# Performance work log

Measured on AMD Instinct MI355X. Metric: run time of the kernel, lower is better.

The kernel has to match this reference:

```python
import jax, jax.numpy as jnp
import numpy as np

ROI = 7      # pooled output size
S = 5        # max adaptive samples per bin dim (boxes <= 0.25*120=30px -> ceil(30/7)=5)


def _roi_align(f, boxes):
    """torchvision roi_align, aligned=True, sampling_ratio=-1 (adaptive).
    f: [C,H,W]; boxes: [N,4] normalized xywh. Returns [N,C,ROI,ROI]."""
    C, H, W = f.shape
    fH, fW = jnp.float32(H), jnp.float32(W)
    x1 = boxes[:, 0] * fW - 0.5                 # aligned=True offset
    y1 = boxes[:, 1] * fH - 0.5
    roi_w = boxes[:, 2] * fW
    roi_h = boxes[:, 3] * fH
    bin_w = roi_w / ROI
    bin_h = roi_h / ROI
    gw = jnp.maximum(jnp.ceil(roi_w / ROI), 1.0)   # adaptive grid counts [N]
    gh = jnp.maximum(jnp.ceil(roi_h / ROI), 1.0)
    ph = jnp.arange(ROI, dtype=jnp.float32)
    s = jnp.arange(S, dtype=jnp.float32)
    # sample coords [N, ROI, S]
    ys = y1[:, None, None] + ph[None, :, None] * bin_h[:, None, None] \
         + (s[None, None, :] + 0.5) * bin_h[:, None, None] / gh[:, None, None]
    xs = x1[:, None, None] + ph[None, :, None] * bin_w[:, None, None] \
         + (s[None, None, :] + 0.5) * bin_w[:, None, None] / gw[:, None, None]
    # broadcast to [N, ROI, ROI, S, S]
    y = ys[:, :, None, :, None]
    x = xs[:, None, :, None, :]
    m = ((s[None, None, None, :, None] < gh[:, None, None, None, None]) &
         (s[None, None, None, None, :] < gw[:, None, None, None, None]))
    valid = (y > -1.0) & (y < fH) & (x > -1.0) & (x < fW)
    yc = jnp.clip(y, 0.0, fH - 1.0)
    xc = jnp.clip(x, 0.0, fW - 1.0)
    y0 = jnp.floor(yc).astype(jnp.int32)
    x0 = jnp.floor(xc).astype(jnp.int32)
    yh = jnp.minimum(y0 + 1, H - 1)
    xh = jnp.minimum(x0 + 1, W - 1)
    ly = yc - y0.astype(jnp.float32); hy = 1.0 - ly
    lx = xc - x0.astype(jnp.float32); hx = 1.0 - lx
    scale = (valid & m).astype(f.dtype)
    y = jnp.broadcast_to(y0 * 0, (boxes.shape[0], ROI, ROI, S, S))  # shape anchor (unused)
    w00 = (hy * hx * scale)[None]
    w01 = (hy * lx * scale)[None]
    w10 = (ly * hx * scale)[None]
    w11 = (ly * lx * scale)[None]
    # gathered values: [C, N, ROI, ROI, S, S]
    vals = (w00 * f[:, y0, x0] + w01 * f[:, y0, xh] +
            w10 * f[:, yh, x0] + w11 * f[:, yh, xh])
    count = (gh * gw)[None, :, None, None]
    pooled = vals.sum(axis=(-1, -2)) / count        # [C, N, ROI, ROI]
    return pooled.transpose(1, 0, 2, 3)              # [N, C, ROI, ROI]


def setup_inputs() -> dict:
    key = jax.random.key(0)
    k = jax.random.split(key, 6)
    features = jax.random.normal(k[0], (1, 128, 120, 120), jnp.float32)
    u = jax.random.uniform(k[1], (512, 4), jnp.float32)
    boxes = jnp.stack([u[:, 0] * 0.7, u[:, 1] * 0.7,
                       0.05 + 0.2 * u[:, 2], 0.05 + 0.2 * u[:, 3]], axis=1)
    d_in = 128 * ROI * ROI  # 6272
    W1 = jax.random.normal(k[2], (d_in, 512), jnp.float32) / np.float32(np.sqrt(d_in))
    b1 = jax.random.normal(k[3], (512,), jnp.float32) * 0.01
    W2 = jax.random.normal(k[4], (512, 256), jnp.float32) / np.float32(np.sqrt(512))
    b2 = jax.random.normal(k[5], (256,), jnp.float32) * 0.01
    return {"features": features, "boxes": boxes, "W1": W1, "b1": b1, "W2": W2, "b2": b2}


def reference(features, boxes, W1, b1, W2, b2):
    roi = _roi_align(features[0], boxes)             # [N,128,7,7]
    flat = roi.reshape(roi.shape[0], -1)             # [N,6272] channel-major like torch .view
    h = jax.nn.relu(flat @ W1 + b1)                  # dropout in eval mode = identity
    return h @ W2 + b2                               # [N,256]
```

## Files before the change

### kernel.cpp

```cpp
#include <hip/hip_runtime.h>
#include <hip/hip_bf16.h>
#include <stdint.h>

#define DI __device__ __forceinline__

typedef __attribute__((ext_vector_type(8))) short short8;
typedef __attribute__((ext_vector_type(4))) float f32x4;

constexpr int CH   = 128;
constexpr int FH   = 120;
constexpr int FW   = 120;
constexpr int NBOX = 512;
constexpr int KDIM = 49 * 128;
constexpr int D1   = 512;
constexpr int D2   = 256;
constexpr int SPLITS = 14;
constexpr int KC     = KDIM / SPLITS;

DI float bf2f(uint32_t u16) { union { uint32_t i; float f; } v; v.i = u16 << 16; return v.f; }
DI float bf2f_hi(uint32_t u) { union { uint32_t i; float f; } v; v.i = u & 0xffff0000u; return v.f; }
DI uint16_t f2bf(float f) {
    __hip_bfloat16 h = __float2bfloat16(f);
    union { __hip_bfloat16 h; uint16_t u; } v; v.h = h; return v.u;
}

__global__ __launch_bounds__(256) void k_pre(const float* __restrict__ f,
                                             const float* __restrict__ W1,
                                             const float* __restrict__ W2,
                                             uint32_t* __restrict__ ft,
                                             uint16_t* __restrict__ W1rT,
                                             uint16_t* __restrict__ W2T) {
    __shared__ __align__(16) char smem[16896];
    const int v = blockIdx.x, t = threadIdx.x;
    if (v < 480) {
        float* lds = (float*)smem;
        const int y = v >> 2, x0 = (v & 3) * 30;
        for (int e = t; e < 30 * 128; e += 256) {
            int c = e / 30, x = e - c * 30;
            lds[x * 129 + c] = f[c * (FH * FW) + y * FW + x0 + x];
        }
        __syncthreads();
        for (int e = t; e < 30 * 64; e += 256) {
            int x = e >> 6, cp = e & 63;
            float lo = lds[x * 129 + 2 * cp];
            float hi = lds[x * 129 + 2 * cp + 1];
            ft[(y * FW + x0 + x) * 64 + cp] = (uint32_t)f2bf(lo) | ((uint32_t)f2bf(hi) << 16);
        }
    } else if (v < 512) {
        float* lds = (float*)smem;
        const int v2 = v - 480;
        const int n0 = (v2 & 7) * 32, k0 = (v2 >> 3) * 128;
        for (int e = t; e < 4096; e += 256) {
            int k = e >> 5, nn = e & 31;
            lds[k * 33 + nn] = W2[(k0 + k) * D2 + n0 + nn];
        }
        __syncthreads();
        for (int e = t; e < 4096; e += 256) {
            int nn = e >> 7, k = e & 127;
            W2T[(n0 + nn) * D1 + k0 + k] = f2bf(lds[k * 33 + nn]);
        }
    } else {
        float* lds = (float*)smem;
        const int vb = v - 512;
        const int b = vb % 49, j0 = (vb / 49) * 32;
        for (int e = t; e < 4096; e += 256) {
            int ci = e >> 5, jj = e & 31;
            lds[ci * 33 + jj] = W1[(ci * 49 + b) * D1 + j0 + jj];
        }
        __syncthreads();
        for (int e = t; e < 4096; e += 256) {
            int jj = e >> 7, ci = e & 127;
            W1rT[(size_t)(j0 + jj) * KDIM + b * 128 + ci] = f2bf(lds[ci * 33 + jj]);
        }
    }
}

__global__ __launch_bounds__(256) void k_roi(const uint32_t* __restrict__ ft,
                                             const float* __restrict__ boxes,
                                             uint32_t* __restrict__ A) {
#pragma clang fp contract(off)
    const int wid  = (blockIdx.x << 2) + (threadIdx.x >> 6);
    const int lane = threadIdx.x & 63;
    const int box = wid / 49, bin = wid % 49;
    const int ph = bin / 7, pw = bin % 7;

    const float bx = boxes[box * 4 + 0], by = boxes[box * 4 + 1];
    const float bw = boxes[box * 4 + 2], bh = boxes[box * 4 + 3];
    const float x1 = bx * 120.0f - 0.5f;
    const float y1 = by * 120.0f - 0.5f;
    const float roi_w = bw * 120.0f, roi_h = bh * 120.0f;
    const float bin_w = roi_w / 7.0f, bin_h = roi_h / 7.0f;
    const float gwf = fmaxf(ceilf(roi_w / 7.0f), 1.0f);
    const float ghf = fmaxf(ceilf(roi_h / 7.0f), 1.0f);
    const int gwi = (int)gwf, ghi = (int)ghf;

    const float ybase = y1 + (float)ph * bin_h;
    const float xbase = x1 + (float)pw * bin_w;

    int offx0[5], offxh[5];
    float hxm[5], lxm[5];
#pragma unroll
    for (int j = 0; j < 5; ++j) {
        float xx = xbase + ((float)j + 0.5f) * bin_w / gwf;
        bool vx = (j < gwi) && (xx > -1.0f) && (xx < 120.0f);
        float xc = fminf(fmaxf(xx, 0.0f), 119.0f);
        int x0 = (int)floorf(xc);
        int xh = min(x0 + 1, 119);
        float lx = xc - (float)x0, hx = 1.0f - lx;
        float mx = vx ? 1.0f : 0.0f;
        hxm[j] = hx * mx; lxm[j] = lx * mx;
        offx0[j] = x0 * 64; offxh[j] = xh * 64;
    }

    float acc0 = 0.0f, acc1 = 0.0f;
    for (int sy = 0; sy < ghi; ++sy) {
        float yy = ybase + ((float)sy + 0.5f) * bin_h / ghf;
        float my = ((yy > -1.0f) && (yy < 120.0f)) ? 1.0f : 0.0f;
        float yc = fminf(fmaxf(yy, 0.0f), 119.0f);
        int y0 = (int)floorf(yc);
        int yh = min(y0 + 1, 119);
        float ly = yc - (float)y0, hy = 1.0f - ly;
        float hym = hy * my, lym = ly * my;
        const uint32_t* r0 = ft + (size_t)(y0 * FW) * 64 + lane;
        const uint32_t* r1 = ft + (size_t)(yh * FW) * 64 + lane;
        uint32_t u00[5], u01[5], u10[5], u11[5];
#pragma unroll
        for (int j = 0; j < 5; ++j) {
            u00[j] = r0[offx0[j]];
            u01[j] = r0[offxh[j]];
            u10[j] = r1[offx0[j]];
            u11[j] = r1[offxh[j]];
        }
#pragma unroll
        for (int j = 0; j < 5; ++j) {
            float w00 = hym * hxm[j], w01 = hym * lxm[j];
            float w10 = lym * hxm[j], w11 = lym * lxm[j];
            acc0 += w00 * bf2f(u00[j] & 0xffffu) + w01 * bf2f(u01[j] & 0xffffu)
                  + w10 * bf2f(u10[j] & 0xffffu) + w11 * bf2f(u11[j] & 0xffffu);
            acc1 += w00 * bf2f_hi(u00[j]) + w01 * bf2f_hi(u01[j])
                  + w10 * bf2f_hi(u10[j]) + w11 * bf2f_hi(u11[j]);
        }
    }
    const float cnt = ghf * gwf;
    const float v0 = acc0 / cnt, v1 = acc1 / cnt;
    A[(size_t)wid * 64 + lane] = (uint32_t)f2bf(v0) | ((uint32_t)f2bf(v1) << 16);
}

__global__ __launch_bounds__(256) void k_gemm1(const uint16_t* __restrict__ A,
                                               const uint16_t* __restrict__ B,
                                               float* __restrict__ P) {
    __shared__ __align__(16) uint16_t As[128 * 32];
    __shared__ __align__(16) uint16_t Bs[128 * 32];
    const int t = threadIdx.x;
    const int lane = t & 63, w = t >> 6;
    const int wr = w >> 1, wc = w & 1;
    const int m0 = blockIdx.x * 128, n0 = blockIdx.y * 128;
    const int kbase = blockIdx.z * KC;

    f32x4 acc[4][4] = {};
    const int kb = lane >> 4, r16 = lane & 15;

    for (int ks = 0; ks < KC / 32; ++ks) {
        const int kk = kbase + ks * 32;
        __syncthreads();
#pragma unroll
        for (int i = 0; i < 2; ++i) {
            int ch = t + 256 * i;
            int row = ch >> 2, c8 = ch & 3;
            int sw = (row >> 1) & 3;
            const uint16_t* ga = A + (size_t)(m0 + row) * KDIM + kk + c8 * 8;
            *(uint4*)&As[row * 32 + (c8 ^ sw) * 8] = *(const uint4*)ga;
            const uint16_t* gb = B + (size_t)(n0 + row) * KDIM + kk + c8 * 8;
            *(uint4*)&Bs[row * 32 + (c8 ^ sw) * 8] = *(const uint4*)gb;
        }
        __syncthreads();

        short8 af[4], bfr[4];
#pragma unroll
        for (int mi = 0; mi < 4; ++mi) {
            int ar = wr * 64 + mi * 16 + r16;
            af[mi] = *(const short8*)&As[ar * 32 + (kb ^ ((ar >> 1) & 3)) * 8];
        }
#pragma unroll
        for (int ni = 0; ni < 4; ++ni) {
            int br = wc * 64 + ni * 16 + r16;
            bfr[ni] = *(const short8*)&Bs[br * 32 + (kb ^ ((br >> 1) & 3)) * 8];
        }
#pragma unroll
        for (int mi = 0; mi < 4; ++mi)
#pragma unroll
            for (int ni = 0; ni < 4; ++ni)
                acc[mi][ni] = __builtin_amdgcn_mfma_f32_16x16x32_bf16(af[mi], bfr[ni], acc[mi][ni], 0, 0, 0);
    }

    float* outp = P + (size_t)blockIdx.z * (D1 * D1);
#pragma unroll
    for (int mi = 0; mi < 4; ++mi)
#pragma unroll
        for (int ni = 0; ni < 4; ++ni) {
            int row = m0 + wr * 64 + mi * 16 + kb * 4;
            int col = n0 + wc * 64 + ni * 16 + r16;
#pragma unroll
            for (int r = 0; r < 4; ++r)
                outp[(size_t)(row + r) * D1 + col] = acc[mi][ni][r];
        }
}

__global__ __launch_bounds__(256) void k_reduce1(const float* __restrict__ P,
                                                 const float* __restrict__ b1,
                                                 uint16_t* __restrict__ Hm) {
    const int e4 = blockIdx.x * 256 + threadIdx.x;
    const f32x4* P4 = (const f32x4*)P;
    f32x4 s = {};
#pragma unroll
    for (int i = 0; i < SPLITS; ++i) s += P4[(size_t)i * (D1 * D1 / 4) + e4];
    const int c4 = (e4 & 127) * 4;
    uint16_t h[4];
#pragma unroll
    for (int j = 0; j < 4; ++j) h[j] = f2bf(fmaxf(s[j] + b1[c4 + j], 0.0f));
    uint2 pk;
    pk.x = (uint32_t)h[0] | ((uint32_t)h[1] << 16);
    pk.y = (uint32_t)h[2] | ((uint32_t)h[3] << 16);
    *(uint2*)&Hm[(size_t)e4 * 4] = pk;
}

__global__ __launch_bounds__(256) void k_gemm2(const uint16_t* __restrict__ Hm,
                                               const uint16_t* __restrict__ W2T,
                                               const float* __restrict__ b2,
                                               float* __restrict__ out) {
    const int wid  = blockIdx.x * 4 + (threadIdx.x >> 6);
    const int lane = threadIdx.x & 63;
    const int mt = wid >> 4, nt = wid & 15;
    const int m0 = mt * 16, n0 = nt * 16;
    const int g = lane >> 4, i = lane & 15;
    f32x4 acc = {};
#pragma unroll
    for (int kk = 0; kk < D1 / 32; ++kk) {
        short8 a = *(const short8*)&Hm[(m0 + i) * D1 + kk * 32 + g * 8];
        short8 b = *(const short8*)&W2T[(n0 + i) * D1 + kk * 32 + g * 8];
        acc = __builtin_amdgcn_mfma_f32_16x16x32_bf16(a, b, acc, 0, 0, 0);
    }
    const float bias = b2[n0 + i];
#pragma unroll
    for (int r = 0; r < 4; ++r)
        out[(size_t)(m0 + g * 4 + r) * D2 + n0 + i] = acc[r] + bias;
}

extern "C" void kernel_launch(void* const* d_in, const int* in_sizes, int n_in,
                              void* d_out, int out_size, void* d_ws, size_t ws_size,
                              hipStream_t stream) {
    const float* f     = (const float*)d_in[0];
    const float* boxes = (const float*)d_in[1];
    const float* W1    = (const float*)d_in[2];
    const float* b1    = (const float*)d_in[3];
    const float* W2    = (const float*)d_in[4];
    const float* b2    = (const float*)d_in[5];
    float* out = (float*)d_out;

    char* p = (char*)d_ws;
    uint32_t* ft   = (uint32_t*)p; p += (size_t)FH * FW * (CH / 2) * 4;
    uint16_t* W1rT = (uint16_t*)p; p += (size_t)D1 * KDIM * 2;
    uint16_t* W2T  = (uint16_t*)p; p += (size_t)D2 * D1 * 2;
    uint16_t* Ar   = (uint16_t*)p; p += (size_t)NBOX * KDIM * 2;
    float*    Pp   = (float*)p;    p += (size_t)SPLITS * D1 * D1 * 4;
    uint16_t* Hm   = (uint16_t*)p; p += (size_t)D1 * D1 * 2;

    k_pre<<<1296, 256, 0, stream>>>(f, W1, W2, ft, W1rT, W2T);
    k_roi<<<(NBOX * 49) / 4, 256, 0, stream>>>(ft, boxes, (uint32_t*)Ar);
    k_gemm1<<<dim3(4, 4, SPLITS), 256, 0, stream>>>(Ar, W1rT, Pp);
    k_reduce1<<<D1 * D1 / 4 / 256, 256, 0, stream>>>(Pp, b1, Hm);
    k_gemm2<<<(D1 / 16) * (D2 / 16) / 4, 256, 0, stream>>>(Hm, W2T, b2, out);
}
```

Measured before the change: 70.70 us.

## Move weight conversion into ROI kernel and fuse split-K reduce into GEMM2

The weight transpose/convert blocks for W1 and W2 move out of the preprocessing kernel and into the ROI-align launch as extra blocks. Preprocessing now only transposes the feature map, which shortens the critical path before ROI sampling. The split-K reduction with bias and ReLU is fused into the second GEMM through LDS, which removes one launch and the Hm round trip to global memory. The fused GEMM2 runs only 32 blocks, so the split-K reduction gets less parallelism than before.

```diff
diff --git a/kernel.cpp b/kernel.cpp
--- a/kernel.cpp
+++ b/kernel.cpp
@@ -24,31 +24,114 @@
     union { __hip_bfloat16 h; uint16_t u; } v; v.h = h; return v.u;
 }
 
-__global__ __launch_bounds__(256) void k_pre(const float* __restrict__ f,
-                                             const float* __restrict__ W1,
-                                             const float* __restrict__ W2,
-                                             uint32_t* __restrict__ ft,
-                                             uint16_t* __restrict__ W1rT,
-                                             uint16_t* __restrict__ W2T) {
-    __shared__ __align__(16) char smem[16896];
+__global__ __launch_bounds__(256) void k_preft(const float* __restrict__ f,
+                                               uint32_t* __restrict__ ft) {
+    __shared__ float lds[30 * 129];
     const int v = blockIdx.x, t = threadIdx.x;
-    if (v < 480) {
-        float* lds = (float*)smem;
-        const int y = v >> 2, x0 = (v & 3) * 30;
-        for (int e = t; e < 30 * 128; e += 256) {
-            int c = e / 30, x = e - c * 30;
-            lds[x * 129 + c] = f[c * (FH * FW) + y * FW + x0 + x];
-        }
-        __syncthreads();
-        for (int e = t; e < 30 * 64; e += 256) {
-            int x = e >> 6, cp = e & 63;
-            float lo = lds[x * 129 + 2 * cp];
-            float hi = lds[x * 129 + 2 * cp + 1];
-            ft[(y * FW + x0 + x) * 64 + cp] = (uint32_t)f2bf(lo) | ((uint32_t)f2bf(hi) << 16);
-        }
-    } else if (v < 512) {
-        float* lds = (float*)smem;
-        const int v2 = v - 480;
+    const int y = v >> 2, x0 = (v & 3) * 30;
+    for (int e = t; e < 30 * 128; e += 256) {
+        int c = e / 30, x = e - c * 30;
+        lds[x * 129 + c] = f[c * (FH * FW) + y * FW + x0 + x];
+    }
+    __syncthreads();
+    for (int e = t; e < 30 * 64; e += 256) {
+        int x = e >> 6, cp = e & 63;
+        float lo = lds[x * 129 + 2 * cp];
+        float hi = lds[x * 129 + 2 * cp + 1];
+        ft[(y * FW + x0 + x) * 64 + cp] = (uint32_t)f2bf(lo) | ((uint32_t)f2bf(hi) << 16);
+    }
+}
+
+__global__ __launch_bounds__(256) void k_roi_w(const uint32_t* __restrict__ ft,
+                                               const float* __restrict__ boxes,
+                                               const float* __restrict__ W1,
+                                               const float* __restrict__ W2,
+                                               uint32_t* __restrict__ A,
+                                               uint16_t* __restrict__ W1rT,
+                                               uint16_t* __restrict__ W2T) {
+    __shared__ __align__(16) float lds[128 * 33];
+    const int blk = blockIdx.x, t = threadIdx.x;
+    if (blk < 6272) {
+#pragma clang fp contract(off)
+        const int wid  = (blk << 2) + (t >> 6);
+        const int lane = t & 63;
+        const int box = wid / 49, bin = wid % 49;
+        const int ph = bin / 7, pw = bin % 7;
+
+        const float bx = boxes[box * 4 + 0], by = boxes[box * 4 + 1];
+        const float bw = boxes[box * 4 + 2], bh = boxes[box * 4 + 3];
+        const float x1 = bx * 120.0f - 0.5f;
+        const float y1 = by * 120.0f - 0.5f;
+        const float roi_w = bw * 120.0f, roi_h = bh * 120.0f;
+        const float bin_w = roi_w / 7.0f, bin_h = roi_h / 7.0f;
+        const float gwf = fmaxf(ceilf(roi_w / 7.0f), 1.0f);
+        const float ghf = fmaxf(ceilf(roi_h / 7.0f), 1.0f);
+        const int gwi = (int)gwf, ghi = (int)ghf;
+
+        const float ybase = y1 + (float)ph * bin_h;
+        const float xbase = x1 + (float)pw * bin_w;
+
+        int offx0[5], offxh[5];
+        float hxm[5], lxm[5];
+#pragma unroll
+        for (int j = 0; j < 5; ++j) {
+            float xx = xbase + ((float)j + 0.5f) * bin_w / gwf;
+            bool vx = (j < gwi) && (xx > -1.0f) && (xx < 120.0f);
+            float xc = fminf(fmaxf(xx, 0.0f), 119.0f);
+            int x0 = (int)floorf(xc);
+            int xh = min(x0 + 1, 119);
+            float lx = xc - (float)x0, hx = 1.0f - lx;
+            float mx = vx ? 1.0f : 0.0f;
+            hxm[j] = hx * mx; lxm[j] = lx * mx;
+            offx0[j] = x0 * 64; offxh[j] = xh * 64;
+        }
+
+        float acc0 = 0.0f, acc1 = 0.0f;
+        for (int sy = 0; sy < ghi; ++sy) {
+            float yy = ybase + ((float)sy + 0.5f) * bin_h / ghf;
+            float my = ((yy > -1.0f) && (yy < 120.0f)) ? 1.0f : 0.0f;
+            float yc = fminf(fmaxf(yy, 0.0f), 119.0f);
+            int y0 = (int)floorf(yc);
+            int yh = min(y0 + 1, 119);
+            float ly = yc - (float)y0, hy = 1.0f - ly;
+            float hym = hy * my, lym = ly * my;
+            const uint32_t* r0 = ft + (size_t)(y0 * FW) * 64 + lane;
+            const uint32_t* r1 = ft + (size_t)(yh * FW) * 64 + lane;
+            uint32_t u00[5], u01[5], u10[5], u11[5];
+#pragma unroll
+            for (int j = 0; j < 5; ++j) {
+                u00[j] = r0[offx0[j]];
+                u01[j] = r0[offxh[j]];
+                u10[j] = r1[offx0[j]];
+                u11[j] = r1[offxh[j]];
+            }
+#pragma unroll
+            for (int j = 0; j < 5; ++j) {
+                float w00 = hym * hxm[j], w01 = hym * lxm[j];
+                float w10 = lym * hxm[j], w11 = lym * lxm[j];
+                acc0 += w00 * bf2f(u00[j] & 0xffffu) + w01 * bf2f(u01[j] & 0xffffu)
+                      + w10 * bf2f(u10[j] & 0xffffu) + w11 * bf2f(u11[j] & 0xffffu);
+                acc1 += w00 * bf2f_hi(u00[j]) + w01 * bf2f_hi(u01[j])
+                      + w10 * bf2f_hi(u10[j]) + w11 * bf2f_hi(u11[j]);
+            }
+        }
+        const float cnt = ghf * gwf;
+        const float v0 = acc0 / cnt, v1 = acc1 / cnt;
+        A[(size_t)wid * 64 + lane] = (uint32_t)f2bf(v0) | ((uint32_t)f2bf(v1) << 16);
+    } else if (blk < 7056) {
+        const int vb = blk - 6272;
+        const int b = vb % 49, j0 = (vb / 49) * 32;
+        for (int e = t; e < 4096; e += 256) {
+            int ci = e >> 5, jj = e & 31;
+            lds[ci * 33 + jj] = W1[(ci * 49 + b) * D1 + j0 + jj];
+        }
+        __syncthreads();
+        for (int e = t; e < 4096; e += 256) {
+            int jj = e >> 7, ci = e & 127;
+            W1rT[(size_t)(j0 + jj) * KDIM + b * 128 + ci] = f2bf(lds[ci * 33 + jj]);
+        }
+    } else {
+        const int v2 = blk - 7056;
         const int n0 = (v2 & 7) * 32, k0 = (v2 >> 3) * 128;
         for (int e = t; e < 4096; e += 256) {
             int k = e >> 5, nn = e & 31;
@@ -59,91 +142,7 @@
             int nn = e >> 7, k = e & 127;
             W2T[(n0 + nn) * D1 + k0 + k] = f2bf(lds[k * 33 + nn]);
         }
-    } else {
-        float* lds = (float*)smem;
-        const int vb = v - 512;
-        const int b = vb % 49, j0 = (vb / 49) * 32;
-        for (int e = t; e < 4096; e += 256) {
-            int ci = e >> 5, jj = e & 31;
-            lds[ci * 33 + jj] = W1[(ci * 49 + b) * D1 + j0 + jj];
-        }
-        __syncthreads();
-        for (int e = t; e < 4096; e += 256) {
-            int jj = e >> 7, ci = e & 127;
-            W1rT[(size_t)(j0 + jj) * KDIM + b * 128 + ci] = f2bf(lds[ci * 33 + jj]);
-        }
-    }
-}
-
-__global__ __launch_bounds__(256) void k_roi(const uint32_t* __restrict__ ft,
-                                             const float* __restrict__ boxes,
-                                             uint32_t* __restrict__ A) {
-#pragma clang fp contract(off)
-    const int wid  = (blockIdx.x << 2) + (threadIdx.x >> 6);
-    const int lane = threadIdx.x & 63;
-    const int box = wid / 49, bin = wid % 49;
-    const int ph = bin / 7, pw = bin % 7;
-
-    const float bx = boxes[box * 4 + 0], by = boxes[box * 4 + 1];
-    const float bw = boxes[box * 4 + 2], bh = boxes[box * 4 + 3];
-    const float x1 = bx * 120.0f - 0.5f;
-    const float y1 = by * 120.0f - 0.5f;
-    const float roi_w = bw * 120.0f, roi_h = bh * 120.0f;
-    const float bin_w = roi_w / 7.0f, bin_h = roi_h / 7.0f;
-    const float gwf = fmaxf(ceilf(roi_w / 7.0f), 1.0f);
-    const float ghf = fmaxf(ceilf(roi_h / 7.0f), 1.0f);
-    const int gwi = (int)gwf, ghi = (int)ghf;
-
-    const float ybase = y1 + (float)ph * bin_h;
-    const float xbase = x1 + (float)pw * bin_w;
-
-    int offx0[5], offxh[5];
-    float hxm[5], lxm[5];
-#pragma unroll
-    for (int j = 0; j < 5; ++j) {
-        float xx = xbase + ((float)j + 0.5f) * bin_w / gwf;
-        bool vx = (j < gwi) && (xx > -1.0f) && (xx < 120.0f);
-        float xc = fminf(fmaxf(xx, 0.0f), 119.0f);
-        int x0 = (int)floorf(xc);
-        int xh = min(x0 + 1, 119);
-        float lx = xc - (float)x0, hx = 1.0f - lx;
-        float mx = vx ? 1.0f : 0.0f;
-        hxm[j] = hx * mx; lxm[j] = lx * mx;
-        offx0[j] = x0 * 64; offxh[j] = xh * 64;
-    }
-
-    float acc0 = 0.0f, acc1 = 0.0f;
-    for (int sy = 0; sy < ghi; ++sy) {
-        float yy = ybase + ((float)sy + 0.5f) * bin_h / ghf;
-        float my = ((yy > -1.0f) && (yy < 120.0f)) ? 1.0f : 0.0f;
-        float yc = fminf(fmaxf(yy, 0.0f), 119.0f);
-        int y0 = (int)floorf(yc);
-        int yh = min(y0 + 1, 119);
-        float ly = yc - (float)y0, hy = 1.0f - ly;
-        float hym = hy * my, lym = ly * my;
-        const uint32_t* r0 = ft + (size_t)(y0 * FW) * 64 + lane;
-        const uint32_t* r1 = ft + (size_t)(yh * FW) * 64 + lane;
-        uint32_t u00[5], u01[5], u10[5], u11[5];
-#pragma unroll
-        for (int j = 0; j < 5; ++j) {
-            u00[j] = r0[offx0[j]];
-            u01[j] = r0[offxh[j]];
-            u10[j] = r1[offx0[j]];
-            u11[j] = r1[offxh[j]];
-        }
-#pragma unroll
-        for (int j = 0; j < 5; ++j) {
-            float w00 = hym * hxm[j], w01 = hym * lxm[j];
-            float w10 = lym * hxm[j], w11 = lym * lxm[j];
-            acc0 += w00 * bf2f(u00[j] & 0xffffu) + w01 * bf2f(u01[j] & 0xffffu)
-                  + w10 * bf2f(u10[j] & 0xffffu) + w11 * bf2f(u11[j] & 0xffffu);
-            acc1 += w00 * bf2f_hi(u00[j]) + w01 * bf2f_hi(u01[j])
-                  + w10 * bf2f_hi(u10[j]) + w11 * bf2f_hi(u11[j]);
-        }
-    }
-    const float cnt = ghf * gwf;
-    const float v0 = acc0 / cnt, v1 = acc1 / cnt;
-    A[(size_t)wid * 64 + lane] = (uint32_t)f2bf(v0) | ((uint32_t)f2bf(v1) << 16);
+    }
 }
 
 __global__ __launch_bounds__(256) void k_gemm1(const uint16_t* __restrict__ A,
@@ -206,44 +205,52 @@
         }
 }
 
-__global__ __launch_bounds__(256) void k_reduce1(const float* __restrict__ P,
-                                                 const float* __restrict__ b1,
-                                                 uint16_t* __restrict__ Hm) {
-    const int e4 = blockIdx.x * 256 + threadIdx.x;
+__global__ __launch_bounds__(512) void k_gemm2f(const float* __restrict__ P,
+                                                const uint16_t* __restrict__ W2T,
+                                                const float* __restrict__ b1,
+                                                const float* __restrict__ b2,
+                                                float* __restrict__ out) {
+    __shared__ __align__(16) uint32_t Hs[16 * 260];
+    const int t = threadIdx.x;
+    const int m0 = blockIdx.x * 16;
+
     const f32x4* P4 = (const f32x4*)P;
-    f32x4 s = {};
-#pragma unroll
-    for (int i = 0; i < SPLITS; ++i) s += P4[(size_t)i * (D1 * D1 / 4) + e4];
-    const int c4 = (e4 & 127) * 4;
-    uint16_t h[4];
-#pragma unroll
-    for (int j = 0; j < 4; ++j) h[j] = f2bf(fmaxf(s[j] + b1[c4 + j], 0.0f));
-    uint2 pk;
-    pk.x = (uint32_t)h[0] | ((uint32_t)h[1] << 16);
-    pk.y = (uint32_t)h[2] | ((uint32_t)h[3] << 16);
-    *(uint2*)&Hm[(size_t)e4 * 4] = pk;
-}
-
-__global__ __launch_bounds__(256) void k_gemm2(const uint16_t* __restrict__ Hm,
-                                               const uint16_t* __restrict__ W2T,
-                                               const float* __restrict__ b2,
-                                               float* __restrict__ out) {
-    const int wid  = blockIdx.x * 4 + (threadIdx.x >> 6);
-    const int lane = threadIdx.x & 63;
-    const int mt = wid >> 4, nt = wid & 15;
-    const int m0 = mt * 16, n0 = nt * 16;
+    for (int G = t; G < 2048; G += 512) {
+        const int row = G >> 7, c4 = G & 127;
+        const f32x4* src = P4 + (size_t)(m0 + row) * 128 + c4;
+        f32x4 s = {};
+#pragma unroll
+        for (int i = 0; i < SPLITS; ++i) s += src[(size_t)i * 65536];
+        f32x4 bb = *(const f32x4*)&b1[c4 * 4];
+        uint16_t h[4];
+#pragma unroll
+        for (int j = 0; j < 4; ++j) h[j] = f2bf(fmaxf(s[j] + bb[j], 0.0f));
+        Hs[row * 260 + c4 * 2 + 0] = (uint32_t)h[0] | ((uint32_t)h[1] << 16);
+        Hs[row * 260 + c4 * 2 + 1] = (uint32_t)h[2] | ((uint32_t)h[3] << 16);
+    }
+    __syncthreads();
+
+    const int w = t >> 6, lane = t & 63;
     const int g = lane >> 4, i = lane & 15;
-    f32x4 acc = {};
-#pragma unroll
-    for (int kk = 0; kk < D1 / 32; ++kk) {
-        short8 a = *(const short8*)&Hm[(m0 + i) * D1 + kk * 32 + g * 8];
-        short8 b = *(const short8*)&W2T[(n0 + i) * D1 + kk * 32 + g * 8];
-        acc = __builtin_amdgcn_mfma_f32_16x16x32_bf16(a, b, acc, 0, 0, 0);
-    }
-    const float bias = b2[n0 + i];
-#pragma unroll
-    for (int r = 0; r < 4; ++r)
-        out[(size_t)(m0 + g * 4 + r) * D2 + n0 + i] = acc[r] + bias;
+    f32x4 acc[2] = {};
+#pragma unroll
+    for (int kk = 0; kk < 16; ++kk) {
+        short8 a = *(const short8*)&Hs[i * 260 + kk * 16 + g * 4];
+#pragma unroll
+        for (int nt = 0; nt < 2; ++nt) {
+            const int n0 = (w * 2 + nt) * 16;
+            short8 b = *(const short8*)&W2T[(n0 + i) * D1 + kk * 32 + g * 8];
+            acc[nt] = __builtin_amdgcn_mfma_f32_16x16x32_bf16(a, b, acc[nt], 0, 0, 0);
+        }
+    }
+#pragma unroll
+    for (int nt = 0; nt < 2; ++nt) {
+        const int n0 = (w * 2 + nt) * 16;
+        const float bias = b2[n0 + i];
+#pragma unroll
+        for (int r = 0; r < 4; ++r)
+            out[(size_t)(m0 + g * 4 + r) * D2 + n0 + i] = acc[nt][r] + bias;
+    }
 }
 
 extern "C" void kernel_launch(void* const* d_in, const int* in_sizes, int n_in,
@@ -263,11 +270,9 @@
     uint16_t* W2T  = (uint16_t*)p; p += (size_t)D2 * D1 * 2;
     uint16_t* Ar   = (uint16_t*)p; p += (size_t)NBOX * KDIM * 2;
     float*    Pp   = (float*)p;    p += (size_t)SPLITS * D1 * D1 * 4;
-    uint16_t* Hm   = (uint16_t*)p; p += (size_t)D1 * D1 * 2;
-
-    k_pre<<<1296, 256, 0, stream>>>(f, W1, W2, ft, W1rT, W2T);
-    k_roi<<<(NBOX * 49) / 4, 256, 0, stream>>>(ft, boxes, (uint32_t*)Ar);
+
+    k_preft<<<480, 256, 0, stream>>>(f, ft);
+    k_roi_w<<<7088, 256, 0, stream>>>(ft, boxes, W1, W2, (uint32_t*)Ar, W1rT, W2T);
     k_gemm1<<<dim3(4, 4, SPLITS), 256, 0, stream>>>(Ar, W1rT, Pp);
-    k_reduce1<<<D1 * D1 / 4 / 256, 256, 0, stream>>>(Pp, b1, Hm);
-    k_gemm2<<<(D1 / 16) * (D2 / 16) / 4, 256, 0, stream>>>(Hm, W2T, b2, out);
-}
+    k_gemm2f<<<32, 512, 0, stream>>>(Pp, W2T, b1, b2, out);
+}
```

Result: slower. 76.57 us (+8.3%).

## Move weight conversion into ROI kernel and specialize ROI sampling by grid width

Applied to the files above, without the earlier changes.

The weight transpose/bf16 conversion blocks move out of the pre-pass and into the ROI-align launch. The pre-pass now only converts the feature map, so the bandwidth-heavy weight conversion can overlap with the latency-bound ROI sampling. The ROI body is templated on the horizontal sample count so only the needed gathers are issued, and the bilinear accumulation uses packed two-float vectors. This adds code size and a switch that may diverge within a block, since each block's waves come from the same or adjacent boxes.

```diff
diff --git a/kernel.cpp b/kernel.cpp
--- a/kernel.cpp
+++ b/kernel.cpp
@@ -6,6 +6,7 @@
 
 typedef __attribute__((ext_vector_type(8))) short short8;
 typedef __attribute__((ext_vector_type(4))) float f32x4;
+typedef __attribute__((ext_vector_type(2))) float f32x2;
 
 constexpr int CH   = 128;
 constexpr int FH   = 120;
@@ -23,86 +24,37 @@
     __hip_bfloat16 h = __float2bfloat16(f);
     union { __hip_bfloat16 h; uint16_t u; } v; v.h = h; return v.u;
 }
-
-__global__ __launch_bounds__(256) void k_pre(const float* __restrict__ f,
-                                             const float* __restrict__ W1,
-                                             const float* __restrict__ W2,
-                                             uint32_t* __restrict__ ft,
-                                             uint16_t* __restrict__ W1rT,
-                                             uint16_t* __restrict__ W2T) {
-    __shared__ __align__(16) char smem[16896];
+DI f32x2 sp2(float s) { f32x2 r; r.x = s; r.y = s; return r; }
+
+__global__ __launch_bounds__(256) void k_preft(const float* __restrict__ f,
+                                               uint32_t* __restrict__ ft) {
+    __shared__ float lds[30 * 129];
     const int v = blockIdx.x, t = threadIdx.x;
-    if (v < 480) {
-        float* lds = (float*)smem;
-        const int y = v >> 2, x0 = (v & 3) * 30;
-        for (int e = t; e < 30 * 128; e += 256) {
-            int c = e / 30, x = e - c * 30;
-            lds[x * 129 + c] = f[c * (FH * FW) + y * FW + x0 + x];
-        }
-        __syncthreads();
-        for (int e = t; e < 30 * 64; e += 256) {
-            int x = e >> 6, cp = e & 63;
-            float lo = lds[x * 129 + 2 * cp];
-            float hi = lds[x * 129 + 2 * cp + 1];
-            ft[(y * FW + x0 + x) * 64 + cp] = (uint32_t)f2bf(lo) | ((uint32_t)f2bf(hi) << 16);
-        }
-    } else if (v < 512) {
-        float* lds = (float*)smem;
-        const int v2 = v - 480;
-        const int n0 = (v2 & 7) * 32, k0 = (v2 >> 3) * 128;
-        for (int e = t; e < 4096; e += 256) {
-            int k = e >> 5, nn = e & 31;
-            lds[k * 33 + nn] = W2[(k0 + k) * D2 + n0 + nn];
-        }
-        __syncthreads();
-        for (int e = t; e < 4096; e += 256) {
-            int nn = e >> 7, k = e & 127;
-            W2T[(n0 + nn) * D1 + k0 + k] = f2bf(lds[k * 33 + nn]);
-        }
-    } else {
-        float* lds = (float*)smem;
-        const int vb = v - 512;
-        const int b = vb % 49, j0 = (vb / 49) * 32;
-        for (int e = t; e < 4096; e += 256) {
-            int ci = e >> 5, jj = e & 31;
-            lds[ci * 33 + jj] = W1[(ci * 49 + b) * D1 + j0 + jj];
-        }
-        __syncthreads();
-        for (int e = t; e < 4096; e += 256) {
-            int jj = e >> 7, ci = e & 127;
-            W1rT[(size_t)(j0 + jj) * KDIM + b * 128 + ci] = f2bf(lds[ci * 33 + jj]);
-        }
-    }
-}
-
-__global__ __launch_bounds__(256) void k_roi(const uint32_t* __restrict__ ft,
-                                             const float* __restrict__ boxes,
-                                             uint32_t* __restrict__ A) {
+    const int y = v >> 2, x0 = (v & 3) * 30;
+    for (int e = t; e < 30 * 128; e += 256) {
+        int c = e / 30, x = e - c * 30;
+        lds[x * 129 + c] = f[c * (FH * FW) + y * FW + x0 + x];
+    }
+    __syncthreads();
+    for (int e = t; e < 30 * 64; e += 256) {
+        int x = e >> 6, cp = e & 63;
+        float lo = lds[x * 129 + 2 * cp];
+        float hi = lds[x * 129 + 2 * cp + 1];
+        ft[(y * FW + x0 + x) * 64 + cp] = (uint32_t)f2bf(lo) | ((uint32_t)f2bf(hi) << 16);
+    }
+}
+
+template<int GW>
+DI void roi_body(const uint32_t* __restrict__ ft, uint32_t* __restrict__ A,
+                 int wid, int lane, float xbase, float bin_w, float gwf,
+                 float ybase, float bin_h, float ghf, int ghi, float cnt) {
 #pragma clang fp contract(off)
-    const int wid  = (blockIdx.x << 2) + (threadIdx.x >> 6);
-    const int lane = threadIdx.x & 63;
-    const int box = wid / 49, bin = wid % 49;
-    const int ph = bin / 7, pw = bin % 7;
-
-    const float bx = boxes[box * 4 + 0], by = boxes[box * 4 + 1];
-    const float bw = boxes[box * 4 + 2], bh = boxes[box * 4 + 3];
-    const float x1 = bx * 120.0f - 0.5f;
-    const float y1 = by * 120.0f - 0.5f;
-    const float roi_w = bw * 120.0f, roi_h = bh * 120.0f;
-    const float bin_w = roi_w / 7.0f, bin_h = roi_h / 7.0f;
-    const float gwf = fmaxf(ceilf(roi_w / 7.0f), 1.0f);
-    const float ghf = fmaxf(ceilf(roi_h / 7.0f), 1.0f);
-    const int gwi = (int)gwf, ghi = (int)ghf;
-
-    const float ybase = y1 + (float)ph * bin_h;
-    const float xbase = x1 + (float)pw * bin_w;
-
-    int offx0[5], offxh[5];
-    float hxm[5], lxm[5];
-#pragma unroll
-    for (int j = 0; j < 5; ++j) {
+    int offx0[GW], offxh[GW];
+    float hxm[GW], lxm[GW];
+#pragma unroll
+    for (int j = 0; j < GW; ++j) {
         float xx = xbase + ((float)j + 0.5f) * bin_w / gwf;
-        bool vx = (j < gwi) && (xx > -1.0f) && (xx < 120.0f);
+        bool vx = (xx > -1.0f) && (xx < 120.0f);
         float xc = fminf(fmaxf(xx, 0.0f), 119.0f);
         int x0 = (int)floorf(xc);
         int xh = min(x0 + 1, 119);
@@ -112,7 +64,7 @@
         offx0[j] = x0 * 64; offxh[j] = xh * 64;
     }
 
-    float acc0 = 0.0f, acc1 = 0.0f;
+    f32x2 acc = {0.0f, 0.0f};
     for (int sy = 0; sy < ghi; ++sy) {
         float yy = ybase + ((float)sy + 0.5f) * bin_h / ghf;
         float my = ((yy > -1.0f) && (yy < 120.0f)) ? 1.0f : 0.0f;
@@ -121,29 +73,92 @@
         int yh = min(y0 + 1, 119);
         float ly = yc - (float)y0, hy = 1.0f - ly;
         float hym = hy * my, lym = ly * my;
-        const uint32_t* r0 = ft + (size_t)(y0 * FW) * 64 + lane;
-        const uint32_t* r1 = ft + (size_t)(yh * FW) * 64 + lane;
-        uint32_t u00[5], u01[5], u10[5], u11[5];
-#pragma unroll
-        for (int j = 0; j < 5; ++j) {
+        const uint32_t* r0 = ft + (size_t)(y0 * (FW * 64)) + lane;
+        const uint32_t* r1 = ft + (size_t)(yh * (FW * 64)) + lane;
+        uint32_t u00[GW], u01[GW], u10[GW], u11[GW];
+#pragma unroll
+        for (int j = 0; j < GW; ++j) {
             u00[j] = r0[offx0[j]];
             u01[j] = r0[offxh[j]];
             u10[j] = r1[offx0[j]];
             u11[j] = r1[offxh[j]];
         }
 #pragma unroll
-        for (int j = 0; j < 5; ++j) {
+        for (int j = 0; j < GW; ++j) {
             float w00 = hym * hxm[j], w01 = hym * lxm[j];
             float w10 = lym * hxm[j], w11 = lym * lxm[j];
-            acc0 += w00 * bf2f(u00[j] & 0xffffu) + w01 * bf2f(u01[j] & 0xffffu)
-                  + w10 * bf2f(u10[j] & 0xffffu) + w11 * bf2f(u11[j] & 0xffffu);
-            acc1 += w00 * bf2f_hi(u00[j]) + w01 * bf2f_hi(u01[j])
-                  + w10 * bf2f_hi(u10[j]) + w11 * bf2f_hi(u11[j]);
-        }
-    }
-    const float cnt = ghf * gwf;
-    const float v0 = acc0 / cnt, v1 = acc1 / cnt;
+            f32x2 v00 = {bf2f(u00[j] & 0xffffu), bf2f_hi(u00[j])};
+            f32x2 v01 = {bf2f(u01[j] & 0xffffu), bf2f_hi(u01[j])};
+            f32x2 v10 = {bf2f(u10[j] & 0xffffu), bf2f_hi(u10[j])};
+            f32x2 v11 = {bf2f(u11[j] & 0xffffu), bf2f_hi(u11[j])};
+            acc += sp2(w00) * v00 + sp2(w01) * v01 + sp2(w10) * v10 + sp2(w11) * v11;
+        }
+    }
+    const float v0 = acc.x / cnt, v1 = acc.y / cnt;
     A[(size_t)wid * 64 + lane] = (uint32_t)f2bf(v0) | ((uint32_t)f2bf(v1) << 16);
+}
+
+__global__ __launch_bounds__(256) void k_roi_w(const uint32_t* __restrict__ ft,
+                                               const float* __restrict__ boxes,
+                                               const float* __restrict__ W1,
+                                               const float* __restrict__ W2,
+                                               uint32_t* __restrict__ A,
+                                               uint16_t* __restrict__ W1rT,
+                                               uint16_t* __restrict__ W2T) {
+    __shared__ __align__(16) float lds[128 * 33];
+    const int blk = blockIdx.x, t = threadIdx.x;
+    if (blk < 6272) {
+#pragma clang fp contract(off)
+        const int wid  = (blk << 2) + (t >> 6);
+        const int lane = t & 63;
+        const int box = wid / 49, bin = wid % 49;
+        const int ph = bin / 7, pw = bin % 7;
+
+        const float bx = boxes[box * 4 + 0], by = boxes[box * 4 + 1];
+        const float bw = boxes[box * 4 + 2], bh = boxes[box * 4 + 3];
+        const float x1 = bx * 120.0f - 0.5f;
+        const float y1 = by * 120.0f - 0.5f;
+        const float roi_w = bw * 120.0f, roi_h = bh * 120.0f;
+        const float bin_w = roi_w / 7.0f, bin_h = roi_h / 7.0f;
+        const float gwf = fmaxf(ceilf(roi_w / 7.0f), 1.0f);
+        const float ghf = fmaxf(ceilf(roi_h / 7.0f), 1.0f);
+        const int gwi = (int)gwf, ghi = (int)ghf;
+        const float ybase = y1 + (float)ph * bin_h;
+        const float xbase = x1 + (float)pw * bin_w;
+        const float cnt = ghf * gwf;
+
+        switch (gwi) {
+        case 1: roi_body<1>(ft, A, wid, lane, xbase, bin_w, gwf, ybase, bin_h, ghf, ghi, cnt); break;
+        case 2: roi_body<2>(ft, A, wid, lane, xbase, bin_w, gwf, ybase, bin_h, ghf, ghi, cnt); break;
+        case 3: roi_body<3>(ft, A, wid, lane, xbase, bin_w, gwf, ybase, bin_h, ghf, ghi, cnt); break;
+        case 4: roi_body<4>(ft, A, wid, lane, xbase, bin_w, gwf, ybase, bin_h, ghf, ghi, cnt); break;
+        default: roi_body<5>(ft, A, wid, lane, xbase, bin_w, gwf, ybase, bin_h, ghf, ghi, cnt); break;
+        }
+    } else if (blk < 7056) {
+        const int vb = blk - 6272;
+        const int b = vb % 49, j0 = (vb / 49) * 32;
+        for (int e = t; e < 4096; e += 256) {
+            int ci = e >> 5, jj = e & 31;
+            lds[ci * 33 + jj] = W1[(ci * 49 + b) * D1 + j0 + jj];
+        }
+        __syncthreads();
+        for (int e = t; e < 4096; e += 256) {
+            int jj = e >> 7, ci = e & 127;
+            W1rT[(size_t)(j0 + jj) * KDIM + b * 128 + ci] = f2bf(lds[ci * 33 + jj]);
+        }
+    } else {
+        const int v2 = blk - 7056;
+        const int n0 = (v2 & 7) * 32, k0 = (v2 >> 3) * 128;
+        for (int e = t; e < 4096; e += 256) {
+            int k = e >> 5, nn = e & 31;
+            lds[k * 33 + nn] = W2[(k0 + k) * D2 + n0 + nn];
+        }
+        __syncthreads();
+        for (int e = t; e < 4096; e += 256) {
+            int nn = e >> 7, k = e & 127;
+            W2T[(n0 + nn) * D1 + k0 + k] = f2bf(lds[k * 33 + nn]);
+        }
+    }
 }
 
 __global__ __launch_bounds__(256) void k_gemm1(const uint16_t* __restrict__ A,
@@ -265,8 +280,8 @@
     float*    Pp   = (float*)p;    p += (size_t)SPLITS * D1 * D1 * 4;
     uint16_t* Hm   = (uint16_t*)p; p += (size_t)D1 * D1 * 2;
 
-    k_pre<<<1296, 256, 0, stream>>>(f, W1, W2, ft, W1rT, W2T);
-    k_roi<<<(NBOX * 49) / 4, 256, 0, stream>>>(ft, boxes, (uint32_t*)Ar);
+    k_preft<<<480, 256, 0, stream>>>(f, ft);
+    k_roi_w<<<7088, 256, 0, stream>>>(ft, boxes, W1, W2, (uint32_t*)Ar, W1rT, W2T);
     k_gemm1<<<dim3(4, 4, SPLITS), 256, 0, stream>>>(Ar, W1rT, Pp);
     k_reduce1<<<D1 * D1 / 4 / 256, 256, 0, stream>>>(Pp, b1, Hm);
     k_gemm2<<<(D1 / 16) * (D2 / 16) / 4, 256, 0, stream>>>(Hm, W2T, b2, out);
```

Result: faster. 64.68 us (-8.5%).
